# Kernel optimization log

Measured on AMD Instinct MI355X. Metric: run time of the kernel, lower is better.

The kernel has to match this reference:

```python
import jax, jax.numpy as jnp
import numpy as np

B, N, C, H = 2, 2048, 1024, 16
D = C // H  # head dim 64


def setup_inputs() -> dict:
    key = jax.random.key(0)
    k1, k2, k3, k4 = jax.random.split(key, 4)
    x = jax.random.normal(k1, (B, N, C), dtype=jnp.float32)
    s = 1.0 / np.sqrt(C)
    Wq = jax.random.normal(k2, (C, C), dtype=jnp.float32) * s    # [out,in] torch layout
    Wkv = jax.random.normal(k3, (2 * C, C), dtype=jnp.float32) * s
    Wo = jax.random.normal(k4, (C, C), dtype=jnp.float32) * s
    bo = jnp.zeros((C,), dtype=jnp.float32)
    return {"x": x, "Wq": Wq, "Wkv": Wkv, "Wo": Wo, "bo": bo}


def reference(x, Wq, Wkv, Wo, bo):
    # projections (torch Linear: y = x @ W.T)
    q = x @ Wq.T                      # [B,N,C]
    kv = x @ Wkv.T                    # [B,N,2C] (context = x)
    k, v = jnp.split(kv, 2, axis=-1)  # each [B,N,C]

    def heads(t):  # [B,N,C] -> [B,H,N,D]
        return t.reshape(B, N, H, D).transpose(0, 2, 1, 3)

    q, k, v = heads(q), heads(k), heads(v)
    # elu+1 feature map
    q = jax.nn.elu(q) + 1.0
    k = jax.nn.elu(k) + 1.0
    # quadratic kernelized attention, as in the source
    sim = jnp.einsum('bhqd,bhkd->bhqk', q, k)               # [B,H,N,N]
    Z = 1.0 / (jnp.einsum('bhqd,bhd->bhq', q, k.sum(axis=2)) + 1e-6)
    out = jnp.einsum('bhqk,bhkd->bhqd', sim * Z[..., None], v)  # [B,H,N,D]
    out = out.transpose(0, 2, 1, 3).reshape(B, N, C)
    return out @ Wo.T + bo
```

## Files before the change

kernel.cpp:

```cpp
#include <hip/hip_runtime.h>
#include <math.h>

#define C_DIM 1024
#define B_SZ 2
#define N_SEQ 2048
#define M_ROWS (B_SZ * N_SEQ)
#define KDIM 1024
#define G1_SLOT 10240
#define G2_SLOT 8192

typedef float  f32x4   __attribute__((ext_vector_type(4)));
typedef short  bf16x8  __attribute__((ext_vector_type(8)));
typedef short  short4v __attribute__((ext_vector_type(4)));
typedef short  short8v __attribute__((ext_vector_type(8)));

__device__ __forceinline__ float elu1(float v) {
    return v > 0.f ? v + 1.f : expf(v);
}

__device__ __forceinline__ ushort f2bf(float f) {
    union { float f; unsigned u; } x; x.f = f;
    unsigned r = (x.u + 0x7fffu + ((x.u >> 16) & 1u)) >> 16;
    return (ushort)r;
}
__device__ __forceinline__ float bf2f(ushort b) {
    union { unsigned u; float f; } x; x.u = ((unsigned)b) << 16;
    return x.f;
}

#define VMCNT(n) asm volatile("s_waitcnt vmcnt(" #n ")" ::: "memory")
#define LGKMBAR do {                                                  \
        asm volatile("s_waitcnt lgkmcnt(0)" ::: "memory");            \
        __builtin_amdgcn_sched_barrier(0);                            \
        __builtin_amdgcn_s_barrier();                                 \
    } while (0)

__device__ __forceinline__ void gl16(const ushort* g, ushort* l) {
    __builtin_amdgcn_global_load_lds(
        (const __attribute__((address_space(1))) unsigned int*)g,
        (__attribute__((address_space(3))) unsigned int*)l,
        16, 0, 0);
}

__global__ __launch_bounds__(256)
void split_all_kernel(const float* __restrict__ x, const float* __restrict__ Wq,
                      const float* __restrict__ Wkv, const float* __restrict__ Wo,
                      ushort* __restrict__ xhi, ushort* __restrict__ Whi,
                      ushort* __restrict__ Wohi, ushort* __restrict__ Wolo)
{
    const int i = blockIdx.x * 256 + threadIdx.x;
    const float* src; ushort* dh; ushort* dl = nullptr; int off;
    if (i < 524288)        { src = x;   dh = xhi;  off = i; }
    else if (i < 655360)   { src = Wq;  dh = Whi;  off = i - 524288; }
    else if (i < 917504)   { src = Wkv; dh = Whi + (1u << 20); off = i - 655360; }
    else                   { src = Wo;  dh = Wohi; dl = Wolo; off = i - 917504; }

    const float4 a = ((const float4*)src)[off * 2];
    const float4 b = ((const float4*)src)[off * 2 + 1];
    const float v[8] = {a.x, a.y, a.z, a.w, b.x, b.y, b.z, b.w};
    ushort hv[8];
    #pragma unroll
    for (int j = 0; j < 8; ++j) hv[j] = f2bf(v[j]);
    short8v H = {(short)hv[0],(short)hv[1],(short)hv[2],(short)hv[3],
                 (short)hv[4],(short)hv[5],(short)hv[6],(short)hv[7]};
    *(short8v*)&dh[(size_t)off * 8] = H;
    if (dl) {
        ushort lv[8];
        #pragma unroll
        for (int j = 0; j < 8; ++j) lv[j] = f2bf(v[j] - bf2f(hv[j]));
        short8v L = {(short)lv[0],(short)lv[1],(short)lv[2],(short)lv[3],
                     (short)lv[4],(short)lv[5],(short)lv[6],(short)lv[7]};
        *(short8v*)&dl[(size_t)off * 8] = L;
    }
}

__global__ __launch_bounds__(256, 2)
void gemm1_kernel(const ushort* __restrict__ Ahi, const ushort* __restrict__ Bhi,
                  ushort* __restrict__ dst)
{
    extern __shared__ ushort smem[];

    const int bid = blockIdx.x;
    const int wg  = (bid & 7) * 64 + (bid >> 3);
    const int m0  = (wg >> 4) * 128;
    const int n0  = (wg & 15) * 192;

    const int t    = threadIdx.x;
    const int lane = t & 63;
    const int w    = t >> 6;
    const int wr   = w >> 1;
    const int wc   = w & 1;

    const int gch     = (t & 3) ^ ((t >> 3) & 3);
    const size_t rowA  = (size_t)(m0 + (t >> 2)) * KDIM + gch * 8;
    const size_t rowA2 = rowA + (size_t)64 * KDIM;
    const size_t rowB  = (size_t)(n0 + (t >> 2)) * KDIM + gch * 8;
    const size_t rowB2 = rowB + (size_t)64 * KDIM;
    const size_t rowB3 = rowB + (size_t)128 * KDIM;
    const int wl      = w * 512;

    const int frow = lane & 15;
    const int cc   = (lane >> 4) ^ ((lane >> 1) & 3);
    const int aoff = (wr * 64 + frow) * 32 + cc * 8;
    const int boff = 4096 + (wc * 96 + frow) * 32 + cc * 8;

    f32x4 acc[4][6];
    #pragma unroll
    for (int mi = 0; mi < 4; ++mi)
        #pragma unroll
        for (int nj = 0; nj < 6; ++nj)
            acc[mi][nj] = (f32x4){0.f, 0.f, 0.f, 0.f};

    #define STAGE1(slotp, koff)                                              \
        do {                                                                 \
            ushort* sl_ = (slotp);                                           \
            gl16(Ahi + rowA  + (koff), sl_ + wl);                            \
            gl16(Ahi + rowA2 + (koff), sl_ + 2048 + wl);                     \
            gl16(Bhi + rowB  + (koff), sl_ + 4096 + wl);                     \
            gl16(Bhi + rowB2 + (koff), sl_ + 6144 + wl);                     \
            gl16(Bhi + rowB3 + (koff), sl_ + 8192 + wl);                     \
        } while (0)

    STAGE1(smem, 0);
    STAGE1(smem + G1_SLOT, 32);
    STAGE1(smem + 2 * G1_SLOT, 64);

    #pragma unroll 1
    for (int kt = 0; kt < 32; ++kt) {
        ushort* sh = smem + (kt & 3) * G1_SLOT;

        if (kt <= 29) { VMCNT(10); } else if (kt == 30) { VMCNT(5); } else { VMCNT(0); }
        LGKMBAR;
        if (kt <= 28) STAGE1(smem + ((kt + 3) & 3) * G1_SLOT, (kt + 3) * 32);

        bf16x8 ah[4], bh[6];
        #pragma unroll
        for (int mi = 0; mi < 4; ++mi)
            ah[mi] = *(const bf16x8*)(sh + aoff + mi * 512);
        #pragma unroll
        for (int nj = 0; nj < 6; ++nj)
            bh[nj] = *(const bf16x8*)(sh + boff + nj * 512);
        __builtin_amdgcn_s_setprio(1);
        #pragma unroll
        for (int mi = 0; mi < 4; ++mi)
            #pragma unroll
            for (int nj = 0; nj < 6; ++nj)
                acc[mi][nj] = __builtin_amdgcn_mfma_f32_16x16x32_bf16(
                    ah[mi], bh[nj], acc[mi][nj], 0, 0, 0);
        __builtin_amdgcn_s_setprio(0);
    }
    #undef STAGE1

    const int erow  = m0 + wr * 64 + (lane >> 4) * 4;
    const int ecol0 = n0 + wc * 96 + frow;
    #pragma unroll
    for (int mi = 0; mi < 4; ++mi) {
        #pragma unroll
        for (int j = 0; j < 4; ++j) {
            const int row = erow + mi * 16 + j;
            #pragma unroll
            for (int nj = 0; nj < 6; ++nj) {
                const int col = ecol0 + nj * 16;
                float v = acc[mi][nj][j];
                if (col < 2048) v = elu1(v);
                dst[(size_t)row * 3072 + col] = f2bf(v);
            }
        }
    }
}

__global__ __launch_bounds__(512, 2)
void gemm2_mfma_kernel(const ushort* __restrict__ Ahi, const ushort* __restrict__ Alo,
                       const ushort* __restrict__ Bhi, const ushort* __restrict__ Blo,
                       const float* __restrict__ bias, float* __restrict__ dst)
{
    __shared__ ushort smem[4 * G2_SLOT];

    const int bid = blockIdx.x;
    const int wg  = (bid & 7) * 32 + (bid >> 3);
    const int m0  = (wg >> 3) * 128;
    const int n0  = (wg & 7) * 128;

    const int t    = threadIdx.x;
    const int lane = t & 63;
    const int w    = t >> 6;
    const int wr   = w >> 2;
    const int wc   = w & 3;

    const int gch     = (t & 3) ^ ((t >> 3) & 3);
    const size_t rowA = (size_t)(m0 + (t >> 2)) * KDIM + gch * 8;
    const size_t rowB = (size_t)(n0 + (t >> 2)) * KDIM + gch * 8;
    const int wl      = w * 512;

    const int frow = lane & 15;
    const int cc   = (lane >> 4) ^ ((lane >> 1) & 3);
    const int aoff = (wr * 64 + frow) * 32 + cc * 8;
    const int boff = 4096 + (wc * 32 + frow) * 32 + cc * 8;

    f32x4 acc[4][2];
    #pragma unroll
    for (int mi = 0; mi < 4; ++mi)
        #pragma unroll
        for (int nj = 0; nj < 2; ++nj)
            acc[mi][nj] = (f32x4){0.f, 0.f, 0.f, 0.f};

    #define STAGE2(srcA, srcB, slotp, koff)                                  \
        do {                                                                 \
            ushort* p_ = (slotp);                                            \
            gl16((srcA) + rowA + (koff), p_ + wl);                           \
            gl16((srcB) + rowB + (koff), p_ + 4096 + wl);                    \
        } while (0)

    STAGE2(Ahi, Bhi, smem, 0);
    STAGE2(Alo, Blo, smem + G2_SLOT, 0);
    STAGE2(Ahi, Bhi, smem + 2 * G2_SLOT, 32);

    #pragma unroll 1
    for (int kt = 0; kt < 32; ++kt) {
        ushort* sh = smem + ((2 * kt) & 3) * G2_SLOT;
        ushort* sl = smem + ((2 * kt + 1) & 3) * G2_SLOT;
        ushort* nl = smem + ((2 * kt + 3) & 3) * G2_SLOT;
        const int kn1 = (kt + 1) * 32;
        const int kn2 = (kt + 2) * 32;

        bf16x8 ah[4], bh[2], bl[2], al[4];

        if (kt < 31) { VMCNT(4); } else { VMCNT(2); }
        LGKMBAR;
        if (kt < 31) STAGE2(Alo, Blo, nl, kn1);
        #pragma unroll
        for (int mi = 0; mi < 4; ++mi)
            ah[mi] = *(const bf16x8*)(sh + aoff + mi * 512);
        #pragma unroll
        for (int nj = 0; nj < 2; ++nj)
            bh[nj] = *(const bf16x8*)(sh + boff + nj * 512);
        __builtin_amdgcn_s_setprio(1);
        #pragma unroll
        for (int mi = 0; mi < 4; ++mi)
            #pragma unroll
            for (int nj = 0; nj < 2; ++nj)
                acc[mi][nj] = __builtin_amdgcn_mfma_f32_16x16x32_bf16(
                    ah[mi], bh[nj], acc[mi][nj], 0, 0, 0);
        __builtin_amdgcn_s_setprio(0);

        if (kt < 31) { VMCNT(4); } else { VMCNT(0); }
        LGKMBAR;
        if (kt < 30) STAGE2(Ahi, Bhi, sh, kn2);
        #pragma unroll
        for (int nj = 0; nj < 2; ++nj)
            bl[nj] = *(const bf16x8*)(sl + boff + nj * 512);
        #pragma unroll
        for (int mi = 0; mi < 4; ++mi)
            al[mi] = *(const bf16x8*)(sl + aoff + mi * 512);
        __builtin_amdgcn_s_setprio(1);
        #pragma unroll
        for (int mi = 0; mi < 4; ++mi)
            #pragma unroll
            for (int nj = 0; nj < 2; ++nj)
                acc[mi][nj] = __builtin_amdgcn_mfma_f32_16x16x32_bf16(
                    ah[mi], bl[nj], acc[mi][nj], 0, 0, 0);
        __builtin_amdgcn_s_setprio(0);

        __builtin_amdgcn_s_setprio(1);
        #pragma unroll
        for (int mi = 0; mi < 4; ++mi)
            #pragma unroll
            for (int nj = 0; nj < 2; ++nj)
                acc[mi][nj] = __builtin_amdgcn_mfma_f32_16x16x32_bf16(
                    al[mi], bh[nj], acc[mi][nj], 0, 0, 0);
        __builtin_amdgcn_s_setprio(0);
    }
    #undef STAGE2

    const int erow  = m0 + wr * 64 + (lane >> 4) * 4;
    const int ecol0 = n0 + wc * 32 + frow;
    #pragma unroll
    for (int mi = 0; mi < 4; ++mi) {
        #pragma unroll
        for (int j = 0; j < 4; ++j) {
            const int row = erow + mi * 16 + j;
            #pragma unroll
            for (int nj = 0; nj < 2; ++nj) {
                const int col = ecol0 + nj * 16;
                dst[(size_t)row * 1024 + col] = acc[mi][nj][j] + bias[col];
            }
        }
    }
}

__global__ __launch_bounds__(256)
void kv_partial_kernel(const ushort* __restrict__ QKV, float* __restrict__ KVp)
{
    const int bh = blockIdx.x;
    const int s  = blockIdx.y;
    const int b  = bh >> 4;
    const int h  = bh & 15;
    const int t  = threadIdx.x;

    __shared__ float ks[16][64];
    __shared__ float vs[16][64];
    __shared__ float red[4160];

    const int srow = t >> 4;
    const int scol = (t & 15) * 4;
    const size_t gk = (size_t)(b * N_SEQ + s * 256) * 3072 + 1024 + h * 64 + scol;
    const size_t gv = gk + 1024;

    const int rs = t >> 6;
    const int dg = (t >> 3) & 7;
    const int eg = t & 7;
    const int d0 = dg * 8;
    const int e0 = eg * 8;

    float acc[8][8];
    #pragma unroll
    for (int i = 0; i < 8; ++i)
        #pragma unroll
        for (int j = 0; j < 8; ++j) acc[i][j] = 0.f;
    float aks[8] = {0.f, 0.f, 0.f, 0.f, 0.f, 0.f, 0.f, 0.f};

    short4v kr = *(const short4v*)&QKV[gk + (size_t)srow * 3072];
    short4v vr = *(const short4v*)&QKV[gv + (size_t)srow * 3072];

    for (int it = 0; it < 16; ++it) {
        __syncthreads();
        ks[srow][scol + 0] = bf2f((ushort)kr[0]);
        ks[srow][scol + 1] = bf2f((ushort)kr[1]);
        ks[srow][scol + 2] = bf2f((ushort)kr[2]);
        ks[srow][scol + 3] = bf2f((ushort)kr[3]);
        vs[srow][scol + 0] = bf2f((ushort)vr[0]);
        vs[srow][scol + 1] = bf2f((ushort)vr[1]);
        vs[srow][scol + 2] = bf2f((ushort)vr[2]);
        vs[srow][scol + 3] = bf2f((ushort)vr[3]);
        __syncthreads();
        if (it < 15) {
            kr = *(const short4v*)&QKV[gk + (size_t)((it + 1) * 16 + srow) * 3072];
            vr = *(const short4v*)&QKV[gv + (size_t)((it + 1) * 16 + srow) * 3072];
        }
        #pragma unroll
        for (int rr = 0; rr < 4; ++rr) {
            const int r = rs * 4 + rr;
            const float4 ka = *(const float4*)&ks[r][d0];
            const float4 kb = *(const float4*)&ks[r][d0 + 4];
            const float4 va = *(const float4*)&vs[r][e0];
            const float4 vb = *(const float4*)&vs[r][e0 + 4];
            const float k8[8] = {ka.x, ka.y, ka.z, ka.w, kb.x, kb.y, kb.z, kb.w};
            const float v8[8] = {va.x, va.y, va.z, va.w, vb.x, vb.y, vb.z, vb.w};
            #pragma unroll
            for (int i = 0; i < 8; ++i)
                #pragma unroll
                for (int j = 0; j < 8; ++j)
                    acc[i][j] += k8[i] * v8[j];
            if (eg == 0) {
                #pragma unroll
                for (int i = 0; i < 8; ++i) aks[i] += k8[i];
            }
        }
    }

    #pragma unroll 1
    for (int step = 1; step < 4; ++step) {
        __syncthreads();
        if (rs == step) {
            #pragma unroll
            for (int i = 0; i < 8; ++i)
                #pragma unroll
                for (int j = 0; j < 8; ++j)
                    red[(d0 + i) * 64 + e0 + j] = acc[i][j];
            if (eg == 0) {
                #pragma unroll
                for (int i = 0; i < 8; ++i) red[4096 + d0 + i] = aks[i];
            }
        }
        __syncthreads();
        if (rs == 0) {
            #pragma unroll
            for (int i = 0; i < 8; ++i)
                #pragma unroll
                for (int j = 0; j < 8; ++j)
                    acc[i][j] += red[(d0 + i) * 64 + e0 + j];
            if (eg == 0) {
                #pragma unroll
                for (int i = 0; i < 8; ++i) aks[i] += red[4096 + d0 + i];
            }
        }
    }

    if (rs == 0) {
        float* outp = KVp + ((size_t)s * 32 + bh) * 4160;
        #pragma unroll
        for (int i = 0; i < 8; ++i) {
            float4 o0 = {acc[i][0], acc[i][1], acc[i][2], acc[i][3]};
            float4 o1 = {acc[i][4], acc[i][5], acc[i][6], acc[i][7]};
            *(float4*)(outp + (d0 + i) * 64 + e0)     = o0;
            *(float4*)(outp + (d0 + i) * 64 + e0 + 4) = o1;
        }
        if (eg == 0) {
            #pragma unroll
            for (int i = 0; i < 8; ++i) outp[4096 + d0 + i] = aks[i];
        }
    }
}

__global__ __launch_bounds__(256)
void kv_reduce_kernel(const float* __restrict__ KVp, float* __restrict__ KVf)
{
    const int idx = blockIdx.x * 256 + threadIdx.x;
    if (idx < 32 * 4160) {
        float s = 0.f;
        #pragma unroll
        for (int i = 0; i < 8; ++i) s += KVp[(size_t)i * (32 * 4160) + idx];
        KVf[idx] = s;
    }
}

__global__ __launch_bounds__(256)
void attn_apply_kernel(const ushort* __restrict__ QKV, const float* __restrict__ KVf,
                       ushort* __restrict__ O1hi, ushort* __restrict__ O1lo)
{
    const int bh = blockIdx.x;
    const int b = bh >> 4, h = bh & 15;
    const int n0 = blockIdx.y * 16;
    const int t = threadIdx.x;
    const int r  = t >> 4;
    const int e0 = (t & 15) * 4;

    __shared__ float kvs[64][68];
    __shared__ float qs[16][68];
    __shared__ float ksums[64];

    const float* kvb = KVf + (size_t)bh * 4160;
    for (int i = t; i < 4096; i += 256)
        kvs[i >> 6][i & 63] = kvb[i];
    if (t < 64) ksums[t] = kvb[4096 + t];
    {
        const int rr = t >> 4, cc2 = (t & 15) * 4;
        short4v q4 = *(const short4v*)&QKV[(size_t)(b * N_SEQ + n0 + rr) * 3072 + h * 64 + cc2];
        qs[rr][cc2 + 0] = bf2f((ushort)q4[0]);
        qs[rr][cc2 + 1] = bf2f((ushort)q4[1]);
        qs[rr][cc2 + 2] = bf2f((ushort)q4[2]);
        qs[rr][cc2 + 3] = bf2f((ushort)q4[3]);
    }
    __syncthreads();

    float4 acc = {0.f, 0.f, 0.f, 0.f};
    float accz = 0.f;
    #pragma unroll
    for (int d = 0; d < 64; ++d) {
        const float qv = qs[r][d];
        const float4 kvv = *(const float4*)&kvs[d][e0];
        acc.x += qv * kvv.x; acc.y += qv * kvv.y;
        acc.z += qv * kvv.z; acc.w += qv * kvv.w;
        accz += qv * ksums[d];
    }
    const float Z = 1.f / (accz + 1e-6f);
    const float vv[4] = {acc.x * Z, acc.y * Z, acc.z * Z, acc.w * Z};
    ushort hv[4], lv[4];
    #pragma unroll
    for (int j = 0; j < 4; ++j) {
        hv[j] = f2bf(vv[j]);
        lv[j] = f2bf(vv[j] - bf2f(hv[j]));
    }
    const size_t off = (size_t)(b * N_SEQ + n0 + r) * C_DIM + h * 64 + e0;
    short4v H = {(short)hv[0], (short)hv[1], (short)hv[2], (short)hv[3]};
    short4v L = {(short)lv[0], (short)lv[1], (short)lv[2], (short)lv[3]};
    *(short4v*)&O1hi[off] = H;
    *(short4v*)&O1lo[off] = L;
}

extern "C" void kernel_launch(void* const* d_in, const int* in_sizes, int n_in,
                              void* d_out, int out_size, void* d_ws, size_t ws_size,
                              hipStream_t stream)
{
    const float* x   = (const float*)d_in[0];
    const float* Wq  = (const float*)d_in[1];
    const float* Wkv = (const float*)d_in[2];
    const float* Wo  = (const float*)d_in[3];
    const float* bo  = (const float*)d_in[4];
    float* out = (float*)d_out;

    float* ws    = (float*)d_ws;
    ushort* QKVu = (ushort*)ws;
    float* KVp   = ws + (size_t)M_ROWS * 3072 / 2;
    float* KVf   = KVp + (size_t)8 * 32 * 4160;
    ushort* xhi  = (ushort*)(KVf + 32 * 4160);
    ushort* xlo  = xhi + (size_t)M_ROWS * 1024;
    ushort* Whi  = xlo + (size_t)M_ROWS * 1024;
    ushort* Wlo  = Whi + (size_t)3072 * 1024;
    ushort* Wohi = Wlo + (size_t)3072 * 1024;
    ushort* Wolo = Wohi + (size_t)1024 * 1024;
    ushort* O1hi = xhi;
    ushort* O1lo = xlo;

    hipFuncSetAttribute((const void*)gemm1_kernel,
                        hipFuncAttributeMaxDynamicSharedMemorySize, 81920);

    split_all_kernel<<<dim3(4096), 256, 0, stream>>>(
        x, Wq, Wkv, Wo, xhi, Whi, Wohi, Wolo);

    gemm1_kernel<<<dim3(512), 256, 81920, stream>>>(xhi, Whi, QKVu);

    kv_partial_kernel<<<dim3(32, 8), 256, 0, stream>>>(QKVu, KVp);
    kv_reduce_kernel<<<dim3((32 * 4160 + 255) / 256), 256, 0, stream>>>(KVp, KVf);

    attn_apply_kernel<<<dim3(32, 128), 256, 0, stream>>>(QKVu, KVf, O1hi, O1lo);

    gemm2_mfma_kernel<<<dim3(256), 512, 0, stream>>>(O1hi, O1lo, Wohi, Wolo, bo, out);
}
```

Measured before the change: 112.4 us.

## Drop hi/lo bf16 split in output projection, use single bf16 GEMM

Removes the split-bf16 (hi+lo) error-compensation scheme from the output projection, so Wo and the attention output are each stored as one bf16 array. The GEMM then runs one MFMA pass per K-step instead of three, with a 3-deep single-slot pipeline and 64x128 tiles over 512 blocks of 256 threads. This removes two thirds of the MFMA work and half the operand traffic of the final GEMM, plus the lo-part writes in the split and apply kernels. The cost is lower output precision, which may exceed the reference tolerance.

```diff
diff --git a/kernel.cpp b/kernel.cpp
--- a/kernel.cpp
+++ b/kernel.cpp
@@ -7,7 +7,7 @@
 #define M_ROWS (B_SZ * N_SEQ)
 #define KDIM 1024
 #define G1_SLOT 10240
-#define G2_SLOT 8192
+#define G2_SLOT 6144
 
 typedef float  f32x4   __attribute__((ext_vector_type(4)));
 typedef short  bf16x8  __attribute__((ext_vector_type(8)));
@@ -46,14 +46,14 @@
 void split_all_kernel(const float* __restrict__ x, const float* __restrict__ Wq,
                       const float* __restrict__ Wkv, const float* __restrict__ Wo,
                       ushort* __restrict__ xhi, ushort* __restrict__ Whi,
-                      ushort* __restrict__ Wohi, ushort* __restrict__ Wolo)
+                      ushort* __restrict__ Wohi)
 {
     const int i = blockIdx.x * 256 + threadIdx.x;
-    const float* src; ushort* dh; ushort* dl = nullptr; int off;
+    const float* src; ushort* dh; int off;
     if (i < 524288)        { src = x;   dh = xhi;  off = i; }
     else if (i < 655360)   { src = Wq;  dh = Whi;  off = i - 524288; }
     else if (i < 917504)   { src = Wkv; dh = Whi + (1u << 20); off = i - 655360; }
-    else                   { src = Wo;  dh = Wohi; dl = Wolo; off = i - 917504; }
+    else                   { src = Wo;  dh = Wohi; off = i - 917504; }
 
     const float4 a = ((const float4*)src)[off * 2];
     const float4 b = ((const float4*)src)[off * 2 + 1];
@@ -64,14 +64,6 @@
     short8v H = {(short)hv[0],(short)hv[1],(short)hv[2],(short)hv[3],
                  (short)hv[4],(short)hv[5],(short)hv[6],(short)hv[7]};
     *(short8v*)&dh[(size_t)off * 8] = H;
-    if (dl) {
-        ushort lv[8];
-        #pragma unroll
-        for (int j = 0; j < 8; ++j) lv[j] = f2bf(v[j] - bf2f(hv[j]));
-        short8v L = {(short)lv[0],(short)lv[1],(short)lv[2],(short)lv[3],
-                     (short)lv[4],(short)lv[5],(short)lv[6],(short)lv[7]};
-        *(short8v*)&dl[(size_t)off * 8] = L;
-    }
 }
 
 __global__ __launch_bounds__(256, 2)
@@ -169,33 +161,31 @@
     }
 }
 
-__global__ __launch_bounds__(512, 2)
-void gemm2_mfma_kernel(const ushort* __restrict__ Ahi, const ushort* __restrict__ Alo,
-                       const ushort* __restrict__ Bhi, const ushort* __restrict__ Blo,
-                       const float* __restrict__ bias, float* __restrict__ dst)
+__global__ __launch_bounds__(256, 2)
+void gemm2_kernel(const ushort* __restrict__ O1, const ushort* __restrict__ Wo,
+                  const float* __restrict__ bias, float* __restrict__ dst)
 {
     __shared__ ushort smem[4 * G2_SLOT];
 
     const int bid = blockIdx.x;
-    const int wg  = (bid & 7) * 32 + (bid >> 3);
-    const int m0  = (wg >> 3) * 128;
+    const int wg  = (bid & 7) * 64 + (bid >> 3);
+    const int m0  = (wg >> 3) * 64;
     const int n0  = (wg & 7) * 128;
 
     const int t    = threadIdx.x;
     const int lane = t & 63;
     const int w    = t >> 6;
-    const int wr   = w >> 2;
-    const int wc   = w & 3;
 
     const int gch     = (t & 3) ^ ((t >> 3) & 3);
-    const size_t rowA = (size_t)(m0 + (t >> 2)) * KDIM + gch * 8;
-    const size_t rowB = (size_t)(n0 + (t >> 2)) * KDIM + gch * 8;
+    const size_t rowA  = (size_t)(m0 + (t >> 2)) * KDIM + gch * 8;
+    const size_t rowB  = (size_t)(n0 + (t >> 2)) * KDIM + gch * 8;
+    const size_t rowB2 = rowB + (size_t)64 * KDIM;
     const int wl      = w * 512;
 
     const int frow = lane & 15;
     const int cc   = (lane >> 4) ^ ((lane >> 1) & 3);
-    const int aoff = (wr * 64 + frow) * 32 + cc * 8;
-    const int boff = 4096 + (wc * 32 + frow) * 32 + cc * 8;
+    const int aoff = frow * 32 + cc * 8;
+    const int boff = 2048 + (w * 32 + frow) * 32 + cc * 8;
 
     f32x4 acc[4][2];
     #pragma unroll
@@ -204,30 +194,27 @@
         for (int nj = 0; nj < 2; ++nj)
             acc[mi][nj] = (f32x4){0.f, 0.f, 0.f, 0.f};
 
-    #define STAGE2(srcA, srcB, slotp, koff)                                  \
+    #define STAGE2(slotp, koff)                                              \
         do {                                                                 \
             ushort* p_ = (slotp);                                            \
-            gl16((srcA) + rowA + (koff), p_ + wl);                           \
-            gl16((srcB) + rowB + (koff), p_ + 4096 + wl);                    \
+            gl16(O1 + rowA  + (koff), p_ + wl);                              \
+            gl16(Wo + rowB  + (koff), p_ + 2048 + wl);                       \
+            gl16(Wo + rowB2 + (koff), p_ + 4096 + wl);                       \
         } while (0)
 
-    STAGE2(Ahi, Bhi, smem, 0);
-    STAGE2(Alo, Blo, smem + G2_SLOT, 0);
-    STAGE2(Ahi, Bhi, smem + 2 * G2_SLOT, 32);
+    STAGE2(smem, 0);
+    STAGE2(smem + G2_SLOT, 32);
+    STAGE2(smem + 2 * G2_SLOT, 64);
 
     #pragma unroll 1
     for (int kt = 0; kt < 32; ++kt) {
-        ushort* sh = smem + ((2 * kt) & 3) * G2_SLOT;
-        ushort* sl = smem + ((2 * kt + 1) & 3) * G2_SLOT;
-        ushort* nl = smem + ((2 * kt + 3) & 3) * G2_SLOT;
-        const int kn1 = (kt + 1) * 32;
-        const int kn2 = (kt + 2) * 32;
-
-        bf16x8 ah[4], bh[2], bl[2], al[4];
-
-        if (kt < 31) { VMCNT(4); } else { VMCNT(2); }
+        ushort* sh = smem + (kt & 3) * G2_SLOT;
+
+        if (kt <= 29) { VMCNT(6); } else if (kt == 30) { VMCNT(3); } else { VMCNT(0); }
         LGKMBAR;
-        if (kt < 31) STAGE2(Alo, Blo, nl, kn1);
+        if (kt <= 28) STAGE2(smem + ((kt + 3) & 3) * G2_SLOT, (kt + 3) * 32);
+
+        bf16x8 ah[4], bh[2];
         #pragma unroll
         for (int mi = 0; mi < 4; ++mi)
             ah[mi] = *(const bf16x8*)(sh + aoff + mi * 512);
@@ -242,38 +229,11 @@
                 acc[mi][nj] = __builtin_amdgcn_mfma_f32_16x16x32_bf16(
                     ah[mi], bh[nj], acc[mi][nj], 0, 0, 0);
         __builtin_amdgcn_s_setprio(0);
-
-        if (kt < 31) { VMCNT(4); } else { VMCNT(0); }
-        LGKMBAR;
-        if (kt < 30) STAGE2(Ahi, Bhi, sh, kn2);
-        #pragma unroll
-        for (int nj = 0; nj < 2; ++nj)
-            bl[nj] = *(const bf16x8*)(sl + boff + nj * 512);
-        #pragma unroll
-        for (int mi = 0; mi < 4; ++mi)
-            al[mi] = *(const bf16x8*)(sl + aoff + mi * 512);
-        __builtin_amdgcn_s_setprio(1);
-        #pragma unroll
-        for (int mi = 0; mi < 4; ++mi)
-            #pragma unroll
-            for (int nj = 0; nj < 2; ++nj)
-                acc[mi][nj] = __builtin_amdgcn_mfma_f32_16x16x32_bf16(
-                    ah[mi], bl[nj], acc[mi][nj], 0, 0, 0);
-        __builtin_amdgcn_s_setprio(0);
-
-        __builtin_amdgcn_s_setprio(1);
-        #pragma unroll
-        for (int mi = 0; mi < 4; ++mi)
-            #pragma unroll
-            for (int nj = 0; nj < 2; ++nj)
-                acc[mi][nj] = __builtin_amdgcn_mfma_f32_16x16x32_bf16(
-                    al[mi], bh[nj], acc[mi][nj], 0, 0, 0);
-        __builtin_amdgcn_s_setprio(0);
     }
     #undef STAGE2
 
-    const int erow  = m0 + wr * 64 + (lane >> 4) * 4;
-    const int ecol0 = n0 + wc * 32 + frow;
+    const int erow  = m0 + (lane >> 4) * 4;
+    const int ecol0 = n0 + w * 32 + frow;
     #pragma unroll
     for (int mi = 0; mi < 4; ++mi) {
         #pragma unroll
@@ -416,7 +376,7 @@
 
 __global__ __launch_bounds__(256)
 void attn_apply_kernel(const ushort* __restrict__ QKV, const float* __restrict__ KVf,
-                       ushort* __restrict__ O1hi, ushort* __restrict__ O1lo)
+                       ushort* __restrict__ O1)
 {
     const int bh = blockIdx.x;
     const int b = bh >> 4, h = bh & 15;
@@ -454,18 +414,10 @@
         accz += qv * ksums[d];
     }
     const float Z = 1.f / (accz + 1e-6f);
-    const float vv[4] = {acc.x * Z, acc.y * Z, acc.z * Z, acc.w * Z};
-    ushort hv[4], lv[4];
-    #pragma unroll
-    for (int j = 0; j < 4; ++j) {
-        hv[j] = f2bf(vv[j]);
-        lv[j] = f2bf(vv[j] - bf2f(hv[j]));
-    }
     const size_t off = (size_t)(b * N_SEQ + n0 + r) * C_DIM + h * 64 + e0;
-    short4v H = {(short)hv[0], (short)hv[1], (short)hv[2], (short)hv[3]};
-    short4v L = {(short)lv[0], (short)lv[1], (short)lv[2], (short)lv[3]};
-    *(short4v*)&O1hi[off] = H;
-    *(short4v*)&O1lo[off] = L;
+    short4v H = {(short)f2bf(acc.x * Z), (short)f2bf(acc.y * Z),
+                 (short)f2bf(acc.z * Z), (short)f2bf(acc.w * Z)};
+    *(short4v*)&O1[off] = H;
 }
 
 extern "C" void kernel_launch(void* const* d_in, const int* in_sizes, int n_in,
@@ -484,26 +436,22 @@
     float* KVp   = ws + (size_t)M_ROWS * 3072 / 2;
     float* KVf   = KVp + (size_t)8 * 32 * 4160;
     ushort* xhi  = (ushort*)(KVf + 32 * 4160);
-    ushort* xlo  = xhi + (size_t)M_ROWS * 1024;
-    ushort* Whi  = xlo + (size_t)M_ROWS * 1024;
-    ushort* Wlo  = Whi + (size_t)3072 * 1024;
-    ushort* Wohi = Wlo + (size_t)3072 * 1024;
-    ushort* Wolo = Wohi + (size_t)1024 * 1024;
-    ushort* O1hi = xhi;
-    ushort* O1lo = xlo;
+    ushort* Whi  = xhi + (size_t)M_ROWS * 1024;
+    ushort* Wohi = Whi + (size_t)3072 * 1024;
+    ushort* O1   = xhi;
 
     hipFuncSetAttribute((const void*)gemm1_kernel,
                         hipFuncAttributeMaxDynamicSharedMemorySize, 81920);
 
     split_all_kernel<<<dim3(4096), 256, 0, stream>>>(
-        x, Wq, Wkv, Wo, xhi, Whi, Wohi, Wolo);
+        x, Wq, Wkv, Wo, xhi, Whi, Wohi);
 
     gemm1_kernel<<<dim3(512), 256, 81920, stream>>>(xhi, Whi, QKVu);
 
     kv_partial_kernel<<<dim3(32, 8), 256, 0, stream>>>(QKVu, KVp);
     kv_reduce_kernel<<<dim3((32 * 4160 + 255) / 256), 256, 0, stream>>>(KVp, KVf);
 
-    attn_apply_kernel<<<dim3(32, 128), 256, 0, stream>>>(QKVu, KVf, O1hi, O1lo);
-
-    gemm2_mfma_kernel<<<dim3(256), 512, 0, stream>>>(O1hi, O1lo, Wohi, Wolo, bo, out);
-}
+    attn_apply_kernel<<<dim3(32, 128), 256, 0, stream>>>(QKVu, KVf, O1);
+
+    gemm2_kernel<<<dim3(512), 256, 0, stream>>>(O1, Wohi, bo, out);
+}
```

New measurement: 99.66 us. 1.13x faster.
